# Optimization experiments

Hardware: AMD Instinct MI355X
Metric: run time of the kernel (lower is better)

The kernel has to match this reference:

```python
import jax, jax.numpy as jnp
import numpy as np

NUM_EMBEDDINGS = 1024
EMBEDDING_DIM = 64
COMMITMENT_COST = 0.1
DECAY = 0.9
EPSILON = 1e-05


def setup_inputs() -> dict:
    key = jax.random.key(0)
    k1, k2, k3 = jax.random.split(key, 3)
    inputs = jax.random.normal(k1, (16, EMBEDDING_DIM, 4096), dtype=jnp.float32)
    embedding_weight = jax.random.normal(k2, (NUM_EMBEDDINGS, EMBEDDING_DIM), dtype=jnp.float32)
    ema_cluster_size = jnp.zeros((NUM_EMBEDDINGS,), dtype=jnp.float32)
    ema_w = jax.random.normal(k3, (NUM_EMBEDDINGS, EMBEDDING_DIM), dtype=jnp.float32)
    return {
        "inputs": inputs,
        "embedding_weight": embedding_weight,
        "ema_cluster_size": ema_cluster_size,
        "ema_w": ema_w,
    }


def reference(inputs, embedding_weight, ema_cluster_size, ema_w):
    K, D = embedding_weight.shape
    # (B, C, L) -> (B, L, C); C == embedding_dim
    x = jnp.transpose(inputs, (0, 2, 1))
    B, L, _ = x.shape
    flat = x.reshape(-1, D)  # [N, D], N = B*L
    N = flat.shape[0]

    distances = (
        jnp.sum(flat * flat, axis=1, keepdims=True)
        + jnp.sum(embedding_weight * embedding_weight, axis=1)
        - 2.0 * (flat @ embedding_weight.T)
    )
    idx = jnp.argmin(distances, axis=1)  # [N] int

    # embedding lookup (equivalent to one-hot @ weight)
    quantized = embedding_weight[idx].reshape(B, L, D)

    # one-hot column sums and scatter-reduction, without materializing [N, K]
    counts = jnp.zeros((K,), dtype=flat.dtype).at[idx].add(1.0)  # sum(encodings, 0)
    dw = jax.ops.segment_sum(flat, idx, num_segments=K)  # encodings^T @ flat_input

    # EMA updates (training path)
    cs = ema_cluster_size * DECAY + (1.0 - DECAY) * counts
    n = jnp.sum(cs)
    cs = (cs + EPSILON) / (n + K * EPSILON) * n
    new_ema_w = ema_w * DECAY + (1.0 - DECAY) * dw
    new_embedding_weight = new_ema_w / cs[:, None]

    # KLDivLoss(batchmean)(softmax(quantized.detach()), softmax(inputs)) over dim=2
    p_in = jax.nn.softmax(jax.lax.stop_gradient(quantized), axis=2)
    p_tgt = jax.nn.softmax(x, axis=2)
    kl = jnp.sum(p_tgt * (jnp.log(p_tgt) - p_in)) / B
    loss = COMMITMENT_COST * kl

    # straight-through estimator
    quantized_st = x + jax.lax.stop_gradient(quantized - x)

    avg_probs = counts / N
    perplexity = jnp.exp(-jnp.sum(avg_probs * jnp.log(avg_probs + 1e-10)))

    out = jnp.transpose(quantized_st, (0, 2, 1))  # back to (B, C, L)
    encoding_indices = idx[:, None]
    return (out, loss, perplexity, new_embedding_weight, encoding_indices)
```

## Files before the change

kernel.cpp:

```cpp
#include <hip/hip_runtime.h>

#define LDIM 4096
#define DDIM 64
#define KCODES 1024
#define BDIM 16
#define NROWS 65536
#define NSLICE 8
#define SLICE_ROWS (NROWS / NSLICE)

typedef __attribute__((ext_vector_type(8))) short short8;
typedef __attribute__((ext_vector_type(16))) float float16v;

__device__ __forceinline__ unsigned int orderf(float f) {
  unsigned int u = __float_as_uint(f);
  return (u & 0x80000000u) ? ~u : (u | 0x80000000u);
}

__device__ __forceinline__ unsigned long long shfl_xor_u64(unsigned long long v, int m) {
  int lo = __shfl_xor((int)(unsigned int)(v & 0xffffffffull), m, 64);
  int hi = __shfl_xor((int)(unsigned int)(v >> 32), m, 64);
  return ((unsigned long long)(unsigned int)hi << 32) | (unsigned int)lo;
}

__device__ __forceinline__ unsigned int bf16_rne(float x) {
  unsigned int u = __float_as_uint(x);
  return (u + 0x7FFFu + ((u >> 16) & 1u)) >> 16;
}

__global__ void prep_kernel(const float* __restrict__ Ew,
                            float* __restrict__ enorm,
                            float* __restrict__ SE,
                            unsigned short* __restrict__ Epk2) {
  int k = blockIdx.x;
  int d = threadIdx.x;
  float v = Ew[k * DDIM + d];
  float n2 = v * v;
  #pragma unroll
  for (int o = 32; o > 0; o >>= 1) n2 += __shfl_xor(n2, o, 64);
  float m = v;
  #pragma unroll
  for (int o = 32; o > 0; o >>= 1) m = fmaxf(m, __shfl_xor(m, o, 64));
  float e = expf(v - m);
  float Z = e;
  #pragma unroll
  for (int o = 32; o > 0; o >>= 1) Z += __shfl_xor(Z, o, 64);
  SE[k * DDIM + d] = e / Z;
  if (d == 0) enorm[k] = n2;

  unsigned int rh = bf16_rne(v);
  float hif = __uint_as_float(rh << 16);
  unsigned int rl = bf16_rne(v - hif);
  int tile = k >> 5, mm = k & 31;
  int s = d >> 4, h = (d >> 3) & 1, j = d & 7;
  int base = tile * 4096 + (h * 32 + mm) * 8 + j;
  Epk2[base + s * 512]        = (unsigned short)rh;
  Epk2[base + (4 + s) * 512]  = (unsigned short)rl;
}

__launch_bounds__(256, 2)
__global__ void argmin_kernel(const float* __restrict__ inp,
                              const unsigned short* __restrict__ Epk2,
                              const float* __restrict__ enorm,
                              int* __restrict__ idx_ws,
                              float* __restrict__ outidx) {
  const int tid = threadIdx.x;
  const int lane = tid & 63;
  const int w = tid >> 6;
  const int half = lane >> 5;
  const int m = lane & 31;
  const int row_base = blockIdx.x * 128 + w * 32;
  const int b = row_base >> 12;
  const int l0 = row_base & 4095;
  const float* xp = inp + (size_t)b * DDIM * LDIM + l0 + m;

  short8 afr[8];
  #pragma unroll
  for (int s = 0; s < 4; s++) {
    #pragma unroll
    for (int j = 0; j < 8; j++) {
      int d = 16 * s + 8 * half + j;
      float x = xp[(size_t)d * LDIM];
      unsigned int rh = bf16_rne(x);
      float hif = __uint_as_float(rh << 16);
      unsigned int rl = bf16_rne(x - hif);
      afr[s][j] = (short)(unsigned short)rh;
      afr[4 + s][j] = (short)(unsigned short)rl;
    }
  }

  float bsc[16];
  int bix[16];
  #pragma unroll
  for (int j = 0; j < 16; j++) { bsc[j] = 1e30f; bix[j] = 0; }

  const unsigned short* eb = Epk2 + lane * 8;

  short8 bA[8], bB[8];
  float enA, enB;

  #pragma unroll
  for (int s = 0; s < 4; s++) {
    bA[s]     = *(const short8*)(eb + s * 512);
    bA[4 + s] = *(const short8*)(eb + 2048 + s * 512);
  }
  enA = enorm[m];

  #pragma unroll 1
  for (int i = 0; i < 16; i++) {
    const int tB = 2 * i + 1;
    {
      const unsigned short* p = eb + tB * 4096;
      #pragma unroll
      for (int s = 0; s < 4; s++) {
        bB[s]     = *(const short8*)(p + s * 512);
        bB[4 + s] = *(const short8*)(p + 2048 + s * 512);
      }
      enB = enorm[tB * 32 + m];
    }
    {
      float16v a0 = {}, a1 = {}, a2 = {};
      #pragma unroll
      for (int s = 0; s < 4; s++) {
        a0 = __builtin_amdgcn_mfma_f32_32x32x16_bf16(afr[s], bA[s], a0, 0, 0, 0);
        a1 = __builtin_amdgcn_mfma_f32_32x32x16_bf16(afr[s], bA[4 + s], a1, 0, 0, 0);
        a2 = __builtin_amdgcn_mfma_f32_32x32x16_bf16(afr[4 + s], bA[s], a2, 0, 0, 0);
      }
      int ci = 2 * i * 32 + m;
      #pragma unroll
      for (int j = 0; j < 16; j++) {
        float sc = fmaf(-2.f, a0[j] + a1[j] + a2[j], enA);
        if (sc < bsc[j]) { bsc[j] = sc; bix[j] = ci; }
      }
    }
    if (i < 15) {
      const unsigned short* p = eb + (2 * i + 2) * 4096;
      #pragma unroll
      for (int s = 0; s < 4; s++) {
        bA[s]     = *(const short8*)(p + s * 512);
        bA[4 + s] = *(const short8*)(p + 2048 + s * 512);
      }
      enA = enorm[(2 * i + 2) * 32 + m];
    }
    {
      float16v a0 = {}, a1 = {}, a2 = {};
      #pragma unroll
      for (int s = 0; s < 4; s++) {
        a0 = __builtin_amdgcn_mfma_f32_32x32x16_bf16(afr[s], bB[s], a0, 0, 0, 0);
        a1 = __builtin_amdgcn_mfma_f32_32x32x16_bf16(afr[s], bB[4 + s], a1, 0, 0, 0);
        a2 = __builtin_amdgcn_mfma_f32_32x32x16_bf16(afr[4 + s], bB[s], a2, 0, 0, 0);
      }
      int ci = tB * 32 + m;
      #pragma unroll
      for (int j = 0; j < 16; j++) {
        float sc = fmaf(-2.f, a0[j] + a1[j] + a2[j], enB);
        if (sc < bsc[j]) { bsc[j] = sc; bix[j] = ci; }
      }
    }
  }

  #pragma unroll
  for (int j = 0; j < 16; j++) {
    unsigned long long key =
        ((unsigned long long)orderf(bsc[j]) << 32) | (unsigned int)bix[j];
    #pragma unroll
    for (int mm = 1; mm < 32; mm <<= 1) {
      unsigned long long o = shfl_xor_u64(key, mm);
      if (o < key) key = o;
    }
    if (m == 0) {
      int row_local = (j & 3) + 8 * (j >> 2) + 4 * half;
      int grow = row_base + row_local;
      int cidx = (int)(key & 0xffffffffull);
      idx_ws[grow] = cidx;
      outidx[grow] = (float)cidx;
    }
  }
}

__launch_bounds__(256)
__global__ void out_kl_kernel(const float* __restrict__ inp,
                              const float* __restrict__ Ew,
                              const float* __restrict__ SE,
                              const int* __restrict__ idx_ws,
                              float* __restrict__ out,
                              float* __restrict__ klacc) {
  __shared__ float Zs[4][64], S1s[4][64], Us[4][64];
  const int tid = threadIdx.x;
  const int c = tid >> 6;
  const int i = tid & 63;
  const int r = blockIdx.x * 64 + i;
  const int b = r >> 12, l = r & 4095;
  const float* xp = inp + (size_t)b * DDIM * LDIM + l;
  float* op = out + (size_t)b * DDIM * LDIM + l;
  const int k = idx_ws[r];
  const float4* Ek4 = (const float4*)(Ew + k * DDIM) + c * 4;
  const float4* Qk4 = (const float4*)(SE + k * DDIM) + c * 4;

  float Z = 0.f, S1 = 0.f, U = 0.f;
  #pragma unroll
  for (int t = 0; t < 4; t++) {
    float ek[4], qk[4];
    *(float4*)ek = Ek4[t];
    *(float4*)qk = Qk4[t];
    #pragma unroll
    for (int u = 0; u < 4; u++) {
      int d = c * 16 + t * 4 + u;
      float x = xp[(size_t)d * LDIM];
      float e = expf(x);
      Z += e;
      S1 += e * x;
      U += e * qk[u];
      op[(size_t)d * LDIM] = ek[u];
    }
  }
  Zs[c][i] = Z; S1s[c][i] = S1; Us[c][i] = U;
  __syncthreads();
  if (tid < 64) {
    float Zt = Zs[0][i] + Zs[1][i] + Zs[2][i] + Zs[3][i];
    float S1t = S1s[0][i] + S1s[1][i] + S1s[2][i] + S1s[3][i];
    float Ut = Us[0][i] + Us[1][i] + Us[2][i] + Us[3][i];
    float kl = (S1t - Ut) / Zt - logf(Zt);
    #pragma unroll
    for (int o = 32; o > 0; o >>= 1) kl += __shfl_xor(kl, o, 64);
    if (i == 0) atomicAdd(klacc, kl);
  }
}

__launch_bounds__(512)
__global__ void dw_partial_kernel(const float* __restrict__ inp,
                                  const int* __restrict__ idx_ws,
                                  float* __restrict__ partial,
                                  float* __restrict__ pcounts) {
  __shared__ float dwp[KCODES];
  __shared__ float cnt[KCODES];
  const int d = blockIdx.x & 63;
  const int slice = blockIdx.x >> 6;
  const int tid = threadIdx.x;
  const bool do_cnt = (d == 0);

  #pragma unroll
  for (int i = 0; i < KCODES / 512; i++) {
    dwp[tid + i * 512] = 0.f;
    cnt[tid + i * 512] = 0.f;
  }
  __syncthreads();

  const int r0 = slice * SLICE_ROWS;
  for (int i = tid; i < SLICE_ROWS; i += 512) {
    int r = r0 + i;
    int b = r >> 12, l = r & 4095;
    float x = inp[(size_t)b * DDIM * LDIM + (size_t)d * LDIM + l];
    int k = idx_ws[r];
    atomicAdd(&dwp[k], x);
    if (do_cnt) atomicAdd(&cnt[k], 1.0f);
  }
  __syncthreads();

  float* dst = partial + ((size_t)slice * 64 + d) * KCODES;
  #pragma unroll
  for (int i = 0; i < KCODES / 512; i++) dst[tid + i * 512] = dwp[tid + i * 512];
  if (do_cnt) {
    float* cd = pcounts + (size_t)slice * KCODES;
    #pragma unroll
    for (int i = 0; i < KCODES / 512; i++) cd[tid + i * 512] = cnt[tid + i * 512];
  }
}

__global__ void csp_kernel(const float* __restrict__ ema_cs,
                           const float* __restrict__ pcounts,
                           float* __restrict__ csp,
                           float* __restrict__ perp_out) {
  __shared__ float red1[16], red2[16];
  int k = threadIdx.x;
  float c = 0.f;
  #pragma unroll
  for (int sl = 0; sl < NSLICE; sl++) c += pcounts[sl * KCODES + k];
  float cs = ema_cs[k] * 0.9f + 0.1f * c;
  float n = cs;
  #pragma unroll
  for (int o = 32; o > 0; o >>= 1) n += __shfl_xor(n, o, 64);
  if ((k & 63) == 0) red1[k >> 6] = n;
  float a = c * (1.0f / 65536.0f);
  float ent = a * logf(a + 1e-10f);
  float es = ent;
  #pragma unroll
  for (int o = 32; o > 0; o >>= 1) es += __shfl_xor(es, o, 64);
  if ((k & 63) == 0) red2[k >> 6] = es;
  __syncthreads();
  if (k == 0) {
    float t1 = 0.f, t2 = 0.f;
    for (int i = 0; i < 16; i++) { t1 += red1[i]; t2 += red2[i]; }
    red1[0] = t1;
    *perp_out = expf(-t2);
  }
  __syncthreads();
  float N = red1[0];
  csp[k] = (cs + 1e-5f) / (N + 1024.0f * 1e-5f) * N;
}

__launch_bounds__(256)
__global__ void reduce_embed_kernel(const float* __restrict__ partial,
                                    const float* __restrict__ emaw,
                                    const float* __restrict__ csp,
                                    const float* __restrict__ klacc,
                                    float* __restrict__ emb_out,
                                    float* __restrict__ loss_out) {
  int i = blockIdx.x * 256 + threadIdx.x;
  int k = i >> 6, d = i & 63;
  float s = 0.f;
  #pragma unroll
  for (int sl = 0; sl < NSLICE; sl++)
    s += partial[((size_t)sl * 64 + d) * KCODES + k];
  float v = fmaf(0.1f, s, emaw[i] * 0.9f);
  emb_out[i] = v / csp[k];
  if (i == 0) *loss_out = 0.1f * (*klacc) * (1.0f / 16.0f);
}

extern "C" void kernel_launch(void* const* d_in, const int* in_sizes, int n_in,
                              void* d_out, int out_size, void* d_ws, size_t ws_size,
                              hipStream_t stream) {
  const float* inp   = (const float*)d_in[0];
  const float* Ew    = (const float*)d_in[1];
  const float* emacs = (const float*)d_in[2];
  const float* emaw  = (const float*)d_in[3];

  float* out      = (float*)d_out;
  float* loss_out = out + 4194304;
  float* perp_out = out + 4194305;
  float* emb_out  = out + 4194306;
  float* idxf_out = out + 4194306 + 65536;

  char* ws = (char*)d_ws;
  int*   idx_ws  = (int*)(ws);
  float* klacc   = (float*)(ws + 262144);
  float* enorm   = (float*)(ws + 266496);
  float* csp     = (float*)(ws + 270592);
  float* SE      = (float*)(ws + 274688);
  unsigned short* Epk2 = (unsigned short*)(ws + 536832);
  float* partial = (float*)(ws + 536832);
  float* pcounts = (float*)(ws + 2633984);

  hipMemsetAsync(ws + 262144, 0, 256, stream);

  prep_kernel<<<KCODES, 64, 0, stream>>>(Ew, enorm, SE, Epk2);
  argmin_kernel<<<512, 256, 0, stream>>>(inp, Epk2, enorm, idx_ws, idxf_out);
  dw_partial_kernel<<<64 * NSLICE, 512, 0, stream>>>(inp, idx_ws, partial, pcounts);
  csp_kernel<<<1, 1024, 0, stream>>>(emacs, pcounts, csp, perp_out);
  out_kl_kernel<<<NROWS / 64, 256, 0, stream>>>(inp, Ew, SE, idx_ws, out, klacc);
  reduce_embed_kernel<<<NROWS / 256, 256, 0, stream>>>(partial, emaw, csp, klacc,
                                                       emb_out, loss_out);
}
```

Measured before the change: 179.2 us.

## Fuse quantized-output write and KL loss into argmin kernel

Moves the straight-through output write and KL-divergence accumulation into the argmin kernel. The input values already loaded for the distance MMA are kept in registers and reused, and the chosen code index is shared through LDS. This removes a separate kernel launch and a second full read of the input. The trade-off is higher register pressure in the argmin kernel (32 extra floats plus softmax accumulators), which could lower occupancy below the declared two blocks per SM.

```diff
diff --git a/kernel.cpp b/kernel.cpp
--- a/kernel.cpp
+++ b/kernel.cpp
@@ -58,11 +58,17 @@
 }
 
 __launch_bounds__(256, 2)
-__global__ void argmin_kernel(const float* __restrict__ inp,
-                              const unsigned short* __restrict__ Epk2,
-                              const float* __restrict__ enorm,
-                              int* __restrict__ idx_ws,
-                              float* __restrict__ outidx) {
+__global__ void argmin_fused_kernel(const float* __restrict__ inp,
+                                    const unsigned short* __restrict__ Epk2,
+                                    const float* __restrict__ enorm,
+                                    const float* __restrict__ Ew,
+                                    const float* __restrict__ SE,
+                                    int* __restrict__ idx_ws,
+                                    float* __restrict__ outidx,
+                                    float* __restrict__ out,
+                                    float* __restrict__ klacc) {
+  __shared__ int kbuf[4][32];
+
   const int tid = threadIdx.x;
   const int lane = tid & 63;
   const int w = tid >> 6;
@@ -72,7 +78,9 @@
   const int b = row_base >> 12;
   const int l0 = row_base & 4095;
   const float* xp = inp + (size_t)b * DDIM * LDIM + l0 + m;
-
+  float* op = out + (size_t)b * DDIM * LDIM + l0 + m;
+
+  float xr[32];
   short8 afr[8];
   #pragma unroll
   for (int s = 0; s < 4; s++) {
@@ -80,6 +88,7 @@
     for (int j = 0; j < 8; j++) {
       int d = 16 * s + 8 * half + j;
       float x = xp[(size_t)d * LDIM];
+      xr[s * 8 + j] = x;
       unsigned int rh = bf16_rne(x);
       float hif = __uint_as_float(rh << 16);
       unsigned int rl = bf16_rne(x - hif);
@@ -173,57 +182,39 @@
       int cidx = (int)(key & 0xffffffffull);
       idx_ws[grow] = cidx;
       outidx[grow] = (float)cidx;
-    }
-  }
-}
-
-__launch_bounds__(256)
-__global__ void out_kl_kernel(const float* __restrict__ inp,
-                              const float* __restrict__ Ew,
-                              const float* __restrict__ SE,
-                              const int* __restrict__ idx_ws,
-                              float* __restrict__ out,
-                              float* __restrict__ klacc) {
-  __shared__ float Zs[4][64], S1s[4][64], Us[4][64];
-  const int tid = threadIdx.x;
-  const int c = tid >> 6;
-  const int i = tid & 63;
-  const int r = blockIdx.x * 64 + i;
-  const int b = r >> 12, l = r & 4095;
-  const float* xp = inp + (size_t)b * DDIM * LDIM + l;
-  float* op = out + (size_t)b * DDIM * LDIM + l;
-  const int k = idx_ws[r];
-  const float4* Ek4 = (const float4*)(Ew + k * DDIM) + c * 4;
-  const float4* Qk4 = (const float4*)(SE + k * DDIM) + c * 4;
-
-  float Z = 0.f, S1 = 0.f, U = 0.f;
-  #pragma unroll
-  for (int t = 0; t < 4; t++) {
-    float ek[4], qk[4];
-    *(float4*)ek = Ek4[t];
-    *(float4*)qk = Qk4[t];
+      kbuf[w][row_local] = cidx;
+    }
+  }
+
+  const int km = kbuf[w][m];
+
+  const float* SEk = SE + km * DDIM + 8 * half;
+  const float* Ewk = Ew + km * DDIM + 8 * half;
+  float Zh = 0.f, S1h = 0.f, Uh = 0.f;
+  #pragma unroll
+  for (int s = 0; s < 4; s++) {
+    float qv[8], ev[8];
+    *(float4*)&qv[0] = *(const float4*)(SEk + 16 * s);
+    *(float4*)&qv[4] = *(const float4*)(SEk + 16 * s + 4);
+    *(float4*)&ev[0] = *(const float4*)(Ewk + 16 * s);
+    *(float4*)&ev[4] = *(const float4*)(Ewk + 16 * s + 4);
     #pragma unroll
-    for (int u = 0; u < 4; u++) {
-      int d = c * 16 + t * 4 + u;
-      float x = xp[(size_t)d * LDIM];
+    for (int j = 0; j < 8; j++) {
+      float x = xr[s * 8 + j];
       float e = expf(x);
-      Z += e;
-      S1 += e * x;
-      U += e * qk[u];
-      op[(size_t)d * LDIM] = ek[u];
-    }
-  }
-  Zs[c][i] = Z; S1s[c][i] = S1; Us[c][i] = U;
-  __syncthreads();
-  if (tid < 64) {
-    float Zt = Zs[0][i] + Zs[1][i] + Zs[2][i] + Zs[3][i];
-    float S1t = S1s[0][i] + S1s[1][i] + S1s[2][i] + S1s[3][i];
-    float Ut = Us[0][i] + Us[1][i] + Us[2][i] + Us[3][i];
-    float kl = (S1t - Ut) / Zt - logf(Zt);
-    #pragma unroll
-    for (int o = 32; o > 0; o >>= 1) kl += __shfl_xor(kl, o, 64);
-    if (i == 0) atomicAdd(klacc, kl);
-  }
+      Zh += e;
+      S1h += e * x;
+      Uh += e * qv[j];
+      op[(size_t)(16 * s + 8 * half + j) * LDIM] = ev[j];
+    }
+  }
+  float Zt = Zh + __shfl_xor(Zh, 32, 64);
+  float S1t = S1h + __shfl_xor(S1h, 32, 64);
+  float Ut = Uh + __shfl_xor(Uh, 32, 64);
+  float kl = (half == 0) ? ((S1t - Ut) / Zt - logf(Zt)) : 0.f;
+  #pragma unroll
+  for (int o = 32; o > 0; o >>= 1) kl += __shfl_xor(kl, o, 64);
+  if (lane == 0) atomicAdd(klacc, kl);
 }
 
 __launch_bounds__(512)
@@ -343,10 +334,10 @@
   hipMemsetAsync(ws + 262144, 0, 256, stream);
 
   prep_kernel<<<KCODES, 64, 0, stream>>>(Ew, enorm, SE, Epk2);
-  argmin_kernel<<<512, 256, 0, stream>>>(inp, Epk2, enorm, idx_ws, idxf_out);
+  argmin_fused_kernel<<<512, 256, 0, stream>>>(inp, Epk2, enorm, Ew, SE,
+                                               idx_ws, idxf_out, out, klacc);
   dw_partial_kernel<<<64 * NSLICE, 512, 0, stream>>>(inp, idx_ws, partial, pcounts);
   csp_kernel<<<1, 1024, 0, stream>>>(emacs, pcounts, csp, perp_out);
-  out_kl_kernel<<<NROWS / 64, 256, 0, stream>>>(inp, Ew, SE, idx_ws, out, klacc);
   reduce_embed_kernel<<<NROWS / 256, 256, 0, stream>>>(partial, emaw, csp, klacc,
                                                        emb_out, loss_out);
 }
```

New measurement: 189.6 us. 1.06x slower.
